# Kernel tuning notes

Hardware: AMD Instinct MI355X
Metric: run time of the kernel (lower is better)

## Reference

```python
import jax, jax.numpy as jnp
import numpy as np
import math

N_HEADS = 12
K1 = 20
K2 = 20


def _pair(hidden, mask4, H, k1, k2):
    # hidden: [b, L, D]; mask4: [b, 1, L, L]
    b, L, D = hidden.shape
    d = D // H
    h = hidden.reshape(b, L, H, d).transpose(0, 2, 1, 3)  # [b,H,L,d]
    scores = jnp.einsum('bhid,bhjd->bhij', h, h) / math.sqrt(d)  # [b,H,L,L]
    scores = scores * mask4
    att = jax.nn.softmax(scores + (1.0 - mask4) * -10000.0, axis=-1) * mask4
    g_score = att.sum(axis=(1, 2))  # [b,L]
    _, g_top = jax.lax.top_k(g_score, k1)  # [b,k1]
    loc = att.sum(axis=1) * (1.0 - jnp.eye(L, dtype=att.dtype))  # zero diagonal
    _, l_top = jax.lax.top_k(loc, k2)  # [b,L,k2]
    idx = jnp.broadcast_to(g_top[:, :, None], (b, k1, k2))
    l_top = jnp.take_along_axis(l_top, idx, axis=1)  # [b,k1,k2]
    return scores, g_top, l_top


def _triplet(hidden, mask, g_top, l_top):
    # hidden: [b,L,D]; mask: [b,L]; g_top: [b,k1]; l_top: [b,k1,k2]; n_heads=1
    b, L, D = hidden.shape
    k1, k2 = l_top.shape[1], l_top.shape[2]
    h = hidden[:, None]  # [b,1,L,D]
    idx1 = jnp.broadcast_to(g_top[:, None, :, None], (b, 1, k1, D))
    h1 = jnp.take_along_axis(h, idx1, axis=2)  # [b,1,k1,D]
    sd = h1[:, :, :, None, :] - h[:, :, None, :, :]  # [b,1,k1,L,D]
    idx2 = jnp.broadcast_to(l_top[:, None, :, :, None], (b, 1, k1, k2, D))
    sd = jnp.take_along_axis(sd, idx2, axis=3)  # [b,1,k1,k2,D]
    nrm = jnp.linalg.norm(sd, axis=-1, keepdims=True)
    nsd = sd / jnp.maximum(nrm, 1e-12)  # F.normalize(p=2, eps=1e-12)
    angle = jnp.einsum('bhijd,bhikd->bhijk', nsd, nsd)  # [b,1,k1,k2,k2]
    m1 = jnp.take_along_axis(mask, g_top, axis=1)  # [b,k1]
    me = (m1[:, :, None] + mask[:, None, :])[:, None, :, :, None]  # [b,1,k1,L,1]
    idx3 = jnp.broadcast_to(l_top[:, None, :, :, None], (b, 1, k1, k2, 1))
    me = jnp.take_along_axis(me, idx3, axis=3)  # [b,1,k1,k2,1]
    amask = (me * me.swapaxes(-2, -1) == 4.0).astype(angle.dtype)  # both valid
    nz = (angle != 0).astype(angle.dtype) * (1.0 - jnp.eye(k2, dtype=angle.dtype))
    amask = amask * nz
    return angle * amask, amask


def setup_inputs() -> dict:
    key = jax.random.key(0)
    k1, k2 = jax.random.split(key)
    b, L, D = 8, 512, 768
    return {
        's_rep': jax.random.normal(k1, (b, L, D), dtype=jnp.float32),
        't_rep': jax.random.normal(k2, (b, L, D), dtype=jnp.float32),
        'attention_mask': jnp.ones((b, L), dtype=jnp.float32),
    }


def reference(s_rep, t_rep, attention_mask):
    b, L, D = s_rep.shape
    k1 = min(K1, L)
    k2 = min(K2, L)
    mext = attention_mask[:, :, None] * attention_mask[:, None, :]  # [b,L,L]
    mask4 = mext[:, None, :, :]  # broadcasts over heads
    s_pair, s_g, s_l = _pair(s_rep, mask4, N_HEADS, k1, k2)
    t_rep_ng = jax.lax.stop_gradient(t_rep)
    t_pair, t_g, t_l = _pair(t_rep_ng, mask4, N_HEADS, k1, k2)
    t_pair = jax.lax.stop_gradient(t_pair)
    denom = N_HEADS * jnp.sum(mext)
    loss_pair = jnp.sum((s_pair - t_pair) ** 2) / denom
    s_angle, s_mask = _triplet(s_rep, attention_mask, t_g, t_l)
    t_angle, t_mask = _triplet(t_rep_ng, attention_mask, t_g, t_l)
    t_angle = jax.lax.stop_gradient(t_angle)
    diff = s_angle - t_angle
    ad = jnp.abs(diff)
    sl1 = jnp.where(ad < 1.0, 0.5 * diff * diff, ad - 0.5)  # smooth_l1, beta=1
    loss_triplet = jnp.sum(sl1) / jnp.sum(s_mask)
    return loss_pair + loss_triplet
```

## Files before the change

kernel.cpp:

```cpp
#include <hip/hip_runtime.h>
#include <hip/hip_bf16.h>
#include <math.h>

#define Bn 8
#define Ln 512
#define Dn 768
#define NHn 12
#define DHn 64
#define K1n 20
#define K2n 20
#define BST 72
#define TROWS 64

#define WS_ACC    0
#define WS_GSCORE 64
#define WS_LOCR   16448
#define WS_GTOP   344128
#define WS_SBF    357568
#define WS_TBF    6649024
#define WS_ZERO_BYTES 344128

typedef __attribute__((ext_vector_type(8))) short bf16x8;
typedef __attribute__((ext_vector_type(4))) float f32x4;

__device__ inline unsigned short f2bf(float x) {
  __hip_bfloat16 h = __float2bfloat16(x);
  return *reinterpret_cast<unsigned short*>(&h);
}
__device__ inline float bf2f(unsigned short u) {
  return __uint_as_float(((unsigned int)u) << 16);
}

__global__ __launch_bounds__(256) void prep_bf16_kernel(
    const float* __restrict__ s, const float* __restrict__ t,
    unsigned short* __restrict__ sbf, unsigned short* __restrict__ tbf) {
  int gid = blockIdx.x * 256 + threadIdx.x;
  int f = gid * 4;
  int col = f % Dn;
  int rb = f / Dn;
  int row = rb & (Ln - 1);
  int b = rb >> 9;
  int h = col >> 6;
  int k = col & 63;
  size_t dst = (((size_t)(b * NHn + h) * Ln + row) * DHn + k);
  float4 vs = *(const float4*)(s + f);
  float4 vt = *(const float4*)(t + f);
  ushort4 us, ut;
  us.x = f2bf(vs.x); us.y = f2bf(vs.y); us.z = f2bf(vs.z); us.w = f2bf(vs.w);
  ut.x = f2bf(vt.x); ut.y = f2bf(vt.y); ut.z = f2bf(vt.z); ut.w = f2bf(vt.w);
  *(ushort4*)(sbf + dst) = us;
  *(ushort4*)(tbf + dst) = ut;
}

__global__ __launch_bounds__(256) void pairA_kernel(
    const unsigned short* __restrict__ sbf, const unsigned short* __restrict__ tbf,
    const float* __restrict__ mask, float* __restrict__ g_score,
    double* __restrict__ acc) {
  const int b = blockIdx.x & 7;
  const int r = blockIdx.x >> 3;
  const int it = r / NHn;
  const int h = r - it * NHn;
  const int tid = threadIdx.x;
  const int w = tid >> 6;
  const int lane = tid & 63;
  const int lr = lane & 15, lg = lane >> 4;

  __shared__ unsigned short Bs[2][TROWS * BST];
  __shared__ unsigned short Bt[2][TROWS * BST];
  __shared__ float Mcol[Ln];
  __shared__ float gcol[Ln];
  __shared__ float wred[4];

  const int s_r0 = tid >> 3;
  const int s_r1 = s_r0 + 32;
  const int s_c = (tid & 7) * 8;

  for (int j = tid; j < Ln; j += 256) {
    Mcol[j] = mask[b * Ln + j];
    gcol[j] = 0.0f;
  }

  const size_t hb = (size_t)(b * NHn + h) * Ln;
  const int rw = it * 64 + w * 16;
  const unsigned short* pas = sbf + (hb + rw + lr) * DHn + lg * 8;
  const unsigned short* pat = tbf + (hb + rw + lr) * DHn + lg * 8;
  bf16x8 sa0 = *(const bf16x8*)pas;
  bf16x8 sa1 = *(const bf16x8*)(pas + 32);
  bf16x8 ta0 = *(const bf16x8*)pat;
  bf16x8 ta1 = *(const bf16x8*)(pat + 32);

  {
    bf16x8 v0 = *(const bf16x8*)(sbf + (hb + s_r0) * DHn + s_c);
    bf16x8 v1 = *(const bf16x8*)(sbf + (hb + s_r1) * DHn + s_c);
    bf16x8 u0 = *(const bf16x8*)(tbf + (hb + s_r0) * DHn + s_c);
    bf16x8 u1 = *(const bf16x8*)(tbf + (hb + s_r1) * DHn + s_c);
    *(bf16x8*)&Bs[0][s_r0 * BST + s_c] = v0;
    *(bf16x8*)&Bs[0][s_r1 * BST + s_c] = v1;
    *(bf16x8*)&Bt[0][s_r0 * BST + s_c] = u0;
    *(bf16x8*)&Bt[0][s_r1 * BST + s_c] = u1;
  }
  __syncthreads();

  float mrow[4];
  #pragma unroll
  for (int q = 0; q < 4; ++q) mrow[q] = Mcol[rw + lg * 4 + q];

  const f32x4 zero4 = {0.0f, 0.0f, 0.0f, 0.0f};
  float lpair = 0.0f;
  float rsum[4] = {0.0f, 0.0f, 0.0f, 0.0f};

  #pragma unroll 1
  for (int t = 0; t < 8; ++t) {
    const int cur = t & 1;
    bf16x8 v0, v1, u0, u1;
    if (t < 7) {
      const int jn = (t + 1) * TROWS;
      v0 = *(const bf16x8*)(sbf + (hb + jn + s_r0) * DHn + s_c);
      v1 = *(const bf16x8*)(sbf + (hb + jn + s_r1) * DHn + s_c);
      u0 = *(const bf16x8*)(tbf + (hb + jn + s_r0) * DHn + s_c);
      u1 = *(const bf16x8*)(tbf + (hb + jn + s_r1) * DHn + s_c);
    }
    #pragma unroll
    for (int c = 0; c < 4; ++c) {
      const int jl = c * 16;
      const int j0 = t * TROWS + jl;
      const unsigned short* pbs = &Bs[cur][(jl + lr) * BST + lg * 8];
      const unsigned short* pbt = &Bt[cur][(jl + lr) * BST + lg * 8];
      bf16x8 sb0 = *(const bf16x8*)pbs;
      bf16x8 sb1 = *(const bf16x8*)(pbs + 32);
      bf16x8 tb0 = *(const bf16x8*)pbt;
      bf16x8 tb1 = *(const bf16x8*)(pbt + 32);
      f32x4 sacc = __builtin_amdgcn_mfma_f32_16x16x32_bf16(sa0, sb0, zero4, 0, 0, 0);
      sacc = __builtin_amdgcn_mfma_f32_16x16x32_bf16(sa1, sb1, sacc, 0, 0, 0);
      f32x4 tacc = __builtin_amdgcn_mfma_f32_16x16x32_bf16(ta0, tb0, zero4, 0, 0, 0);
      tacc = __builtin_amdgcn_mfma_f32_16x16x32_bf16(ta1, tb1, tacc, 0, 0, 0);
      const float mj = Mcol[j0 + lr];
      #pragma unroll
      for (int q = 0; q < 4; ++q) {
        const float mm = mrow[q] * mj;
        const float ss = sacc[q] * 0.125f * mm;
        const float st = tacc[q] * 0.125f * mm;
        const float d = ss - st;
        lpair += d * d;
        rsum[q] += __expf(st + (1.0f - mm) * (-10000.0f));
      }
    }
    if (t < 7) {
      const int nxt = cur ^ 1;
      *(bf16x8*)&Bs[nxt][s_r0 * BST + s_c] = v0;
      *(bf16x8*)&Bs[nxt][s_r1 * BST + s_c] = v1;
      *(bf16x8*)&Bt[nxt][s_r0 * BST + s_c] = u0;
      *(bf16x8*)&Bt[nxt][s_r1 * BST + s_c] = u1;
    }
    __syncthreads();
  }

  #pragma unroll
  for (int o = 1; o < 16; o <<= 1) {
    #pragma unroll
    for (int q = 0; q < 4; ++q) rsum[q] += __shfl_xor(rsum[q], o, 64);
  }
  float rscale[4];
  #pragma unroll
  for (int q = 0; q < 4; ++q)
    rscale[q] = mrow[q] / fmaxf(rsum[q], 1e-30f);

  {
    bf16x8 u0 = *(const bf16x8*)(tbf + (hb + s_r0) * DHn + s_c);
    bf16x8 u1 = *(const bf16x8*)(tbf + (hb + s_r1) * DHn + s_c);
    *(bf16x8*)&Bt[0][s_r0 * BST + s_c] = u0;
    *(bf16x8*)&Bt[0][s_r1 * BST + s_c] = u1;
  }
  __syncthreads();

  #pragma unroll 1
  for (int t = 0; t < 8; ++t) {
    const int cur = t & 1;
    bf16x8 u0, u1;
    if (t < 7) {
      const int jn = (t + 1) * TROWS;
      u0 = *(const bf16x8*)(tbf + (hb + jn + s_r0) * DHn + s_c);
      u1 = *(const bf16x8*)(tbf + (hb + jn + s_r1) * DHn + s_c);
    }
    #pragma unroll
    for (int c = 0; c < 4; ++c) {
      const int jl = c * 16;
      const int j0 = t * TROWS + jl;
      const unsigned short* pbt = &Bt[cur][(jl + lr) * BST + lg * 8];
      bf16x8 tb0 = *(const bf16x8*)pbt;
      bf16x8 tb1 = *(const bf16x8*)(pbt + 32);
      f32x4 tacc = __builtin_amdgcn_mfma_f32_16x16x32_bf16(ta0, tb0, zero4, 0, 0, 0);
      tacc = __builtin_amdgcn_mfma_f32_16x16x32_bf16(ta1, tb1, tacc, 0, 0, 0);
      const float mj = Mcol[j0 + lr];
      float pc = 0.0f;
      #pragma unroll
      for (int q = 0; q < 4; ++q) {
        const float mm = mrow[q] * mj;
        const float st = tacc[q] * 0.125f * mm;
        const float e = __expf(st + (1.0f - mm) * (-10000.0f));
        pc += e * rscale[q];
      }
      pc += __shfl_xor(pc, 16, 64);
      pc += __shfl_xor(pc, 32, 64);
      if (lg == 0) atomicAdd(&gcol[j0 + lr], pc);
    }
    if (t < 7) {
      const int nxt = cur ^ 1;
      *(bf16x8*)&Bt[nxt][s_r0 * BST + s_c] = u0;
      *(bf16x8*)&Bt[nxt][s_r1 * BST + s_c] = u1;
    }
    __syncthreads();
  }

  #pragma unroll
  for (int o = 1; o < 64; o <<= 1) lpair += __shfl_xor(lpair, o, 64);
  if (lane == 0) wred[w] = lpair;
  __syncthreads();

  if (tid == 0) {
    atomicAdd(&acc[0], (double)((wred[0] + wred[1]) + (wred[2] + wred[3])));
  }
  {
    const int j0 = tid, j1 = tid + 256;
    atomicAdd(&g_score[b * Ln + j0], gcol[j0] * Mcol[j0]);
    atomicAdd(&g_score[b * Ln + j1], gcol[j1] * Mcol[j1]);
  }
}

__global__ __launch_bounds__(256, 4) void pairB_kernel(
    const unsigned short* __restrict__ tbf, const float* __restrict__ mask,
    const float* __restrict__ g_score, int* __restrict__ g_top,
    float* __restrict__ loc_rows) {
  const int b = blockIdx.x & 7;
  const int h = blockIdx.x >> 3;
  const int tid = threadIdx.x;
  const int w = tid >> 6, lane = tid & 63;
  const int lr = lane & 15, lg = lane >> 4;
  const int cw = w * 128;

  __shared__ int gidx[32];
  __shared__ float mrow_s[32];
  __shared__ float rscale_s[32];
  __shared__ float redsum[4][32];
  __shared__ float McolB[Ln];
  __shared__ unsigned short es[32][Ln + 8];

  for (int j = tid; j < Ln; j += 256) McolB[j] = mask[b * Ln + j];
  if (w == 1 && lane < 32 - K1n) gidx[K1n + lane] = 0;
  if (w == 0) {
    float v[8];
    #pragma unroll
    for (int q = 0; q < 8; ++q) v[q] = g_score[b * Ln + q * 64 + lane];
    for (int r = 0; r < K1n; ++r) {
      float bv = v[0]; int bq = 0;
      #pragma unroll
      for (int q = 1; q < 8; ++q) if (v[q] > bv) { bv = v[q]; bq = q; }
      int bj = bq * 64 + lane;
      #pragma unroll
      for (int o = 1; o < 64; o <<= 1) {
        float ov = __shfl_xor(bv, o, 64);
        int oj = __shfl_xor(bj, o, 64);
        if (ov > bv || (ov == bv && oj < bj)) { bv = ov; bj = oj; }
      }
      if (lane == 0) {
        gidx[r] = bj;
        if (h == 0) g_top[b * K1n + r] = bj;
      }
      const int wq = bj >> 6, wl = bj & 63;
      #pragma unroll
      for (int q = 0; q < 8; ++q)
        if (q == wq && lane == wl) v[q] = -3.0e38f;
    }
  }
  __syncthreads();
  if (tid < 32) mrow_s[tid] = (tid < K1n) ? McolB[gidx[tid]] : 0.0f;
  __syncthreads();

  const size_t hb = (size_t)(b * NHn + h) * Ln;
  bf16x8 ta[2][2];
  #pragma unroll
  for (int rt = 0; rt < 2; ++rt) {
    const unsigned short* p = tbf + (hb + gidx[rt * 16 + lr]) * DHn + lg * 8;
    ta[rt][0] = *(const bf16x8*)p;
    ta[rt][1] = *(const bf16x8*)(p + 32);
  }
  const f32x4 zero4 = {0.0f, 0.0f, 0.0f, 0.0f};
  float rsum[2][4] = {{0, 0, 0, 0}, {0, 0, 0, 0}};
  #pragma unroll 1
  for (int ct = 0; ct < 8; ++ct) {
    const int j0 = cw + ct * 16;
    const unsigned short* pb = tbf + (hb + j0 + lr) * DHn + lg * 8;
    bf16x8 tb0 = *(const bf16x8*)pb;
    bf16x8 tb1 = *(const bf16x8*)(pb + 32);
    const float mj = McolB[j0 + lr];
    #pragma unroll
    for (int rt = 0; rt < 2; ++rt) {
      f32x4 tacc = __builtin_amdgcn_mfma_f32_16x16x32_bf16(ta[rt][0], tb0, zero4, 0, 0, 0);
      tacc = __builtin_amdgcn_mfma_f32_16x16x32_bf16(ta[rt][1], tb1, tacc, 0, 0, 0);
      #pragma unroll
      for (int q = 0; q < 4; ++q) {
        const int ri = rt * 16 + lg * 4 + q;
        const float mm = mrow_s[ri] * mj;
        const float st = tacc[q] * 0.125f * mm;
        const float e = __expf(st + (1.0f - mm) * (-10000.0f));
        rsum[rt][q] += e;
        es[ri][j0 + lr] = f2bf(e);
      }
    }
  }
  #pragma unroll
  for (int o = 1; o < 16; o <<= 1) {
    #pragma unroll
    for (int rt = 0; rt < 2; ++rt)
      #pragma unroll
      for (int q = 0; q < 4; ++q) rsum[rt][q] += __shfl_xor(rsum[rt][q], o, 64);
  }
  if (lr == 0) {
    #pragma unroll
    for (int rt = 0; rt < 2; ++rt)
      #pragma unroll
      for (int q = 0; q < 4; ++q) redsum[w][rt * 16 + lg * 4 + q] = rsum[rt][q];
  }
  __syncthreads();
  if (tid < 32) {
    const float fs = redsum[0][tid] + redsum[1][tid] + redsum[2][tid] + redsum[3][tid];
    rscale_s[tid] = mrow_s[tid] / fmaxf(fs, 1e-30f);
  }
  __syncthreads();
  for (int idx = tid; idx < K1n * Ln; idx += 256) {
    const int ri = idx >> 9, j = idx & (Ln - 1);
    const float e = bf2f(es[ri][j]);
    atomicAdd(&loc_rows[(size_t)(b * K1n + ri) * Ln + j], e * rscale_s[ri] * McolB[j]);
  }
}

#define TP (Dn + 16)

__global__ __launch_bounds__(256, 1) void triplet_kernel(
    const float* __restrict__ s_rep, const float* __restrict__ t_rep,
    const float* __restrict__ mask, const int* __restrict__ g_top,
    const float* __restrict__ loc_rows, double* __restrict__ acc,
    unsigned int* __restrict__ done_cnt, float* __restrict__ out) {
  const int blk = blockIdx.x, tid = threadIdx.x;
  const int b = blk / K1n, i1 = blk % K1n;
  const int w = tid >> 6, lane = tid & 63;
  const int lr = lane & 15, lg = lane >> 4;

  __shared__ unsigned short NS[32][TP];
  __shared__ unsigned short NT[32][TP];
  __shared__ int lidx[K2n];
  __shared__ float fl2[K2n];
  __shared__ float sred[4], cred[4];
  __shared__ int is_last;
  __shared__ float red[4];

  const int g = g_top[b * K1n + i1];
  if (w == 0) {
    const float* r0 = loc_rows + (size_t)(b * K1n + i1) * Ln;
    float v[8];
    #pragma unroll
    for (int q = 0; q < 8; ++q) {
      const int j = q * 64 + lane;
      v[q] = (j == g) ? 0.0f : r0[j];
    }
    for (int r = 0; r < K2n; ++r) {
      float bv = v[0]; int bq = 0;
      #pragma unroll
      for (int q = 1; q < 8; ++q) if (v[q] > bv) { bv = v[q]; bq = q; }
      int bj = bq * 64 + lane;
      #pragma unroll
      for (int o = 1; o < 64; o <<= 1) {
        float ov = __shfl_xor(bv, o, 64);
        int oj = __shfl_xor(bj, o, 64);
        if (ov > bv || (ov == bv && oj < bj)) { bv = ov; bj = oj; }
      }
      if (lane == 0) lidx[r] = bj;
      const int wq = bj >> 6, wl = bj & 63;
      #pragma unroll
      for (int q = 0; q < 8; ++q)
        if (q == wq && lane == wl) v[q] = -3.0e38f;
    }
  }
  __syncthreads();
  if (tid < K2n)
    fl2[tid] = (mask[b * Ln + g] + mask[b * Ln + lidx[tid]] == 2.0f) ? 1.0f : 0.0f;
  __syncthreads();

  const float* pgs = s_rep + (size_t)(b * Ln + g) * Dn;
  const float* pgt = t_rep + (size_t)(b * Ln + g) * Dn;
  for (int j = w; j < K2n; j += 4) {
    const float* pls = s_rep + (size_t)(b * Ln + lidx[j]) * Dn;
    const float* plt = t_rep + (size_t)(b * Ln + lidx[j]) * Dn;
    float4 ds[3], dt[3];
    float ssq = 0.0f, tsq = 0.0f;
    #pragma unroll
    for (int q = 0; q < 3; ++q) {
      const int c = lane * 4 + q * 256;
      float4 a = *(const float4*)&pgs[c];
      float4 x = *(const float4*)&pls[c];
      ds[q] = make_float4(a.x - x.x, a.y - x.y, a.z - x.z, a.w - x.w);
      ssq += ds[q].x * ds[q].x + ds[q].y * ds[q].y + ds[q].z * ds[q].z + ds[q].w * ds[q].w;
      float4 c2 = *(const float4*)&pgt[c];
      float4 y = *(const float4*)&plt[c];
      dt[q] = make_float4(c2.x - y.x, c2.y - y.y, c2.z - y.z, c2.w - y.w);
      tsq += dt[q].x * dt[q].x + dt[q].y * dt[q].y + dt[q].z * dt[q].z + dt[q].w * dt[q].w;
    }
    #pragma unroll
    for (int o = 1; o < 64; o <<= 1) {
      ssq += __shfl_xor(ssq, o, 64);
      tsq += __shfl_xor(tsq, o, 64);
    }
    const float sinv = 1.0f / fmaxf(sqrtf(ssq), 1e-12f);
    const float tinv = 1.0f / fmaxf(sqrtf(tsq), 1e-12f);
    #pragma unroll
    for (int q = 0; q < 3; ++q) {
      const int c = lane * 4 + q * 256;
      ushort4 us, ut;
      us.x = f2bf(ds[q].x * sinv); us.y = f2bf(ds[q].y * sinv);
      us.z = f2bf(ds[q].z * sinv); us.w = f2bf(ds[q].w * sinv);
      ut.x = f2bf(dt[q].x * tinv); ut.y = f2bf(dt[q].y * tinv);
      ut.z = f2bf(dt[q].z * tinv); ut.w = f2bf(dt[q].w * tinv);
      *(ushort4*)&NS[j][c] = us;
      *(ushort4*)&NT[j][c] = ut;
    }
  }
  __syncthreads();

  const int qr = w >> 1, qc = w & 1;
  f32x4 sacc = {0.0f, 0.0f, 0.0f, 0.0f};
  f32x4 tacc = {0.0f, 0.0f, 0.0f, 0.0f};
  #pragma unroll
  for (int ks = 0; ks < 24; ++ks) {
    const int kk = ks * 32 + lg * 8;
    bf16x8 as = *(const bf16x8*)&NS[qr * 16 + lr][kk];
    bf16x8 bs = *(const bf16x8*)&NS[qc * 16 + lr][kk];
    bf16x8 at = *(const bf16x8*)&NT[qr * 16 + lr][kk];
    bf16x8 bt = *(const bf16x8*)&NT[qc * 16 + lr][kk];
    sacc = __builtin_amdgcn_mfma_f32_16x16x32_bf16(as, bs, sacc, 0, 0, 0);
    tacc = __builtin_amdgcn_mfma_f32_16x16x32_bf16(at, bt, tacc, 0, 0, 0);
  }
  float psum = 0.0f, pcnt = 0.0f;
  #pragma unroll
  for (int q = 0; q < 4; ++q) {
    const int j2 = qr * 16 + lg * 4 + q;
    const int k2 = qc * 16 + lr;
    if (j2 < K2n && k2 < K2n && j2 != k2) {
      const float am = fl2[j2] * fl2[k2];
      const bool smv = (am != 0.0f) && (sacc[q] != 0.0f);
      const bool tmv = (am != 0.0f) && (tacc[q] != 0.0f);
      const float sv = smv ? sacc[q] : 0.0f;
      const float tv = tmv ? tacc[q] : 0.0f;
      const float d = sv - tv;
      const float ad = fabsf(d);
      psum += (ad < 1.0f) ? 0.5f * d * d : (ad - 0.5f);
      pcnt += smv ? 1.0f : 0.0f;
    }
  }
  #pragma unroll
  for (int o = 1; o < 64; o <<= 1) {
    psum += __shfl_xor(psum, o, 64);
    pcnt += __shfl_xor(pcnt, o, 64);
  }
  if (lane == 0) { sred[w] = psum; cred[w] = pcnt; }
  __syncthreads();
  if (tid == 0) {
    atomicAdd(&acc[1], (double)(sred[0] + sred[1] + sred[2] + sred[3]));
    atomicAdd(&acc[2], (double)(cred[0] + cred[1] + cred[2] + cred[3]));
    __threadfence();
    const unsigned int done = atomicAdd(done_cnt, 1u);
    is_last = (done == (unsigned int)(Bn * K1n - 1)) ? 1 : 0;
  }
  __syncthreads();

  if (is_last) {
    double sm = 0.0;
    for (int bb = 0; bb < Bn; ++bb) {
      float p = 0.0f;
      for (int i = tid; i < Ln; i += 256) p += mask[bb * Ln + i];
      #pragma unroll
      for (int o = 1; o < 64; o <<= 1) p += __shfl_xor(p, o, 64);
      __syncthreads();
      if ((tid & 63) == 0) red[tid >> 6] = p;
      __syncthreads();
      if (tid == 0) {
        float rs = red[0] + red[1] + red[2] + red[3];
        sm += (double)rs * (double)rs;
      }
    }
    __syncthreads();
    if (tid == 0) {
      const double a0 = atomicAdd(&acc[0], 0.0);
      const double a1 = atomicAdd(&acc[1], 0.0);
      const double a2 = atomicAdd(&acc[2], 0.0);
      const double lp = a0 / ((double)NHn * sm);
      const double lt = a1 / a2;
      out[0] = (float)(lp + lt);
    }
  }
}

extern "C" void kernel_launch(void* const* d_in, const int* in_sizes, int n_in,
                              void* d_out, int out_size, void* d_ws, size_t ws_size,
                              hipStream_t stream) {
  const float* s_rep = (const float*)d_in[0];
  const float* t_rep = (const float*)d_in[1];
  const float* mask  = (const float*)d_in[2];
  float* out = (float*)d_out;

  char* w = (char*)d_ws;
  double* acc      = (double*)(w + WS_ACC);
  unsigned int* done_cnt = (unsigned int*)(w + WS_ACC + 48);
  float* g_score   = (float*)(w + WS_GSCORE);
  float* loc_rows  = (float*)(w + WS_LOCR);
  int* g_top       = (int*)(w + WS_GTOP);
  unsigned short* sbf = (unsigned short*)(w + WS_SBF);
  unsigned short* tbf = (unsigned short*)(w + WS_TBF);

  hipMemsetAsync(d_ws, 0, WS_ZERO_BYTES, stream);

  prep_bf16_kernel<<<Bn * Ln * Dn / 4 / 256, 256, 0, stream>>>(s_rep, t_rep, sbf, tbf);
  pairA_kernel<<<Bn * NHn * (Ln / 64), 256, 0, stream>>>(sbf, tbf, mask, g_score, acc);
  pairB_kernel<<<Bn * NHn, 256, 0, stream>>>(tbf, mask, g_score, g_top, loc_rows);
  triplet_kernel<<<Bn * K1n, 256, 0, stream>>>(s_rep, t_rep, mask, g_top, loc_rows,
                                               acc, done_cnt, out);
}
```

Measured before the change: 108.4 us.

## Replace loc_rows atomics with per-head partials and drop workspace memset

pairB now writes each head's local-attention rows to a separate partial buffer with plain stores instead of float atomicAdd into a shared buffer. The triplet kernel sums the 12 head partials when it loads its row. The hipMemsetAsync is removed; block 0 of the prep kernel now zeroes the accumulators and g_score instead. This removes atomic contention and one memset launch, at the cost of a larger workspace and 12 times more reads in the triplet top-k load.

```diff
diff --git a/kernel.cpp b/kernel.cpp
--- a/kernel.cpp
+++ b/kernel.cpp
@@ -14,11 +14,10 @@
 
 #define WS_ACC    0
 #define WS_GSCORE 64
-#define WS_LOCR   16448
-#define WS_GTOP   344128
-#define WS_SBF    357568
-#define WS_TBF    6649024
-#define WS_ZERO_BYTES 344128
+#define WS_GTOP   16448
+#define WS_LOCP   17152
+#define WS_SBF    3949312
+#define WS_TBF    10240768
 
 typedef __attribute__((ext_vector_type(8))) short bf16x8;
 typedef __attribute__((ext_vector_type(4))) float f32x4;
@@ -33,8 +32,14 @@
 
 __global__ __launch_bounds__(256) void prep_bf16_kernel(
     const float* __restrict__ s, const float* __restrict__ t,
-    unsigned short* __restrict__ sbf, unsigned short* __restrict__ tbf) {
-  int gid = blockIdx.x * 256 + threadIdx.x;
+    unsigned short* __restrict__ sbf, unsigned short* __restrict__ tbf,
+    float* __restrict__ g_score, int* __restrict__ accw) {
+  int tid = threadIdx.x;
+  if (blockIdx.x == 0) {
+    if (tid < 16) accw[tid] = 0;
+    for (int i = tid; i < Bn * Ln; i += 256) g_score[i] = 0.0f;
+  }
+  int gid = blockIdx.x * 256 + tid;
   int f = gid * 4;
   int col = f % Dn;
   int rb = f / Dn;
@@ -230,7 +235,7 @@
 __global__ __launch_bounds__(256, 4) void pairB_kernel(
     const unsigned short* __restrict__ tbf, const float* __restrict__ mask,
     const float* __restrict__ g_score, int* __restrict__ g_top,
-    float* __restrict__ loc_rows) {
+    float* __restrict__ loc_part) {
   const int b = blockIdx.x & 7;
   const int h = blockIdx.x >> 3;
   const int tid = threadIdx.x;
@@ -327,10 +332,11 @@
     rscale_s[tid] = mrow_s[tid] / fmaxf(fs, 1e-30f);
   }
   __syncthreads();
+  float* lp = loc_part + (size_t)(h * Bn + b) * K1n * Ln;
   for (int idx = tid; idx < K1n * Ln; idx += 256) {
     const int ri = idx >> 9, j = idx & (Ln - 1);
     const float e = bf2f(es[ri][j]);
-    atomicAdd(&loc_rows[(size_t)(b * K1n + ri) * Ln + j], e * rscale_s[ri] * McolB[j]);
+    lp[idx] = e * rscale_s[ri] * McolB[j];
   }
 }
 
@@ -339,7 +345,7 @@
 __global__ __launch_bounds__(256, 1) void triplet_kernel(
     const float* __restrict__ s_rep, const float* __restrict__ t_rep,
     const float* __restrict__ mask, const int* __restrict__ g_top,
-    const float* __restrict__ loc_rows, double* __restrict__ acc,
+    const float* __restrict__ loc_part, double* __restrict__ acc,
     unsigned int* __restrict__ done_cnt, float* __restrict__ out) {
   const int blk = blockIdx.x, tid = threadIdx.x;
   const int b = blk / K1n, i1 = blk % K1n;
@@ -356,12 +362,16 @@
 
   const int g = g_top[b * K1n + i1];
   if (w == 0) {
-    const float* r0 = loc_rows + (size_t)(b * K1n + i1) * Ln;
+    const float* r0 = loc_part + (size_t)(b * K1n + i1) * Ln;
     float v[8];
     #pragma unroll
     for (int q = 0; q < 8; ++q) {
       const int j = q * 64 + lane;
-      v[q] = (j == g) ? 0.0f : r0[j];
+      float sv = 0.0f;
+      #pragma unroll
+      for (int hh = 0; hh < NHn; ++hh)
+        sv += r0[(size_t)hh * Bn * K1n * Ln + j];
+      v[q] = (j == g) ? 0.0f : sv;
     }
     for (int r = 0; r < K2n; ++r) {
       float bv = v[0]; int bq = 0;
@@ -511,16 +521,15 @@
   double* acc      = (double*)(w + WS_ACC);
   unsigned int* done_cnt = (unsigned int*)(w + WS_ACC + 48);
   float* g_score   = (float*)(w + WS_GSCORE);
-  float* loc_rows  = (float*)(w + WS_LOCR);
   int* g_top       = (int*)(w + WS_GTOP);
+  float* loc_part  = (float*)(w + WS_LOCP);
   unsigned short* sbf = (unsigned short*)(w + WS_SBF);
   unsigned short* tbf = (unsigned short*)(w + WS_TBF);
 
-  hipMemsetAsync(d_ws, 0, WS_ZERO_BYTES, stream);
-
-  prep_bf16_kernel<<<Bn * Ln * Dn / 4 / 256, 256, 0, stream>>>(s_rep, t_rep, sbf, tbf);
+  prep_bf16_kernel<<<Bn * Ln * Dn / 4 / 256, 256, 0, stream>>>(
+      s_rep, t_rep, sbf, tbf, g_score, (int*)(w + WS_ACC));
   pairA_kernel<<<Bn * NHn * (Ln / 64), 256, 0, stream>>>(sbf, tbf, mask, g_score, acc);
-  pairB_kernel<<<Bn * NHn, 256, 0, stream>>>(tbf, mask, g_score, g_top, loc_rows);
-  triplet_kernel<<<Bn * K1n, 256, 0, stream>>>(s_rep, t_rep, mask, g_top, loc_rows,
+  pairB_kernel<<<Bn * NHn, 256, 0, stream>>>(tbf, mask, g_score, g_top, loc_part);
+  triplet_kernel<<<Bn * K1n, 256, 0, stream>>>(s_rep, t_rep, mask, g_top, loc_part,
                                                acc, done_cnt, out);
 }
```

After: 103.2 us. 1.05x faster.
